# Optimization experiments

Measured on AMD Instinct MI355X. Metric: run time of the kernel, lower is better.

## Reference

```python
import jax, jax.numpy as jnp
import numpy as np

N_NODES = 50000

def _sage(x, src, dst, Wl, bl, Wr):
    # PyG SAGEConv(aggr='mean'): out = lin_l(mean_{j in N(i)} x_j) + lin_r(x_i)
    msg = x[src]                                                    # [E, F] gather
    agg = jax.ops.segment_sum(msg, dst, num_segments=N_NODES)      # [N, F]
    cnt = jax.ops.segment_sum(jnp.ones((src.shape[0],), x.dtype), dst, num_segments=N_NODES)
    agg = agg / jnp.maximum(cnt, 1.0)[:, None]                     # mean aggregate
    return agg @ Wl + bl + x @ Wr                                   # lin_l has bias, lin_r does not


def setup_inputs() -> dict:
    key = jax.random.key(0)
    ks = jax.random.split(key, 14)
    d_in, d_h, d_out, n_edges = 128, 64, 4, 800000
    s = lambda k, shp, fan: jax.random.normal(k, shp, jnp.float32) * (1.0 / np.sqrt(fan))
    return {
        'x': jax.random.normal(ks[0], (N_NODES, d_in), jnp.float32),
        'edge_index': jax.random.randint(ks[1], (2, n_edges), 0, N_NODES, jnp.int64),
        'Wl1': s(ks[2], (d_in, d_h), d_in), 'bl1': jnp.zeros((d_h,), jnp.float32),
        'Wr1': s(ks[3], (d_in, d_h), d_in),
        'Wl2': s(ks[4], (d_h, d_h), d_h), 'bl2': jnp.zeros((d_h,), jnp.float32),
        'Wr2': s(ks[5], (d_h, d_h), d_h),
        'Wl3': s(ks[6], (d_h, d_h), d_h), 'bl3': jnp.zeros((d_h,), jnp.float32),
        'Wr3': s(ks[7], (d_h, d_h), d_h),
        'Wp': s(ks[8], (2 * d_h, d_out), 2 * d_h), 'bp': jnp.zeros((d_out,), jnp.float32),
    }


def reference(x, edge_index, Wl1, bl1, Wr1, Wl2, bl2, Wr2, Wl3, bl3, Wr3, Wp, bp):
    src, dst = edge_index[0], edge_index[1]
    # dropout is identity in eval mode
    h = jax.nn.elu(_sage(x, src, dst, Wl1, bl1, Wr1))
    h = jax.nn.elu(_sage(h, src, dst, Wl2, bl2, Wr2))
    h = jax.nn.elu(_sage(h, src, dst, Wl3, bl3, Wr3))
    edge_feat = jnp.concatenate([h[src], h[dst]], axis=1)  # [E, 2*hidden]
    return edge_feat @ Wp + bp                              # [E, output_dim]
```

## Files before the change

kernel.cpp:

```cpp
#include <hip/hip_runtime.h>
#include <hip/hip_bf16.h>

#define N_NODES 50000
#define N_EDGES 800000
#define D_IN 128
#define D_H 64
#define SCAN_BLOCKS 196
#define HIST_BLOCKS 3125
#define LIN1_BLOCKS 782

#define F1L 0
#define F1R 8192
#define F2L 16384
#define F2R 20480
#define F3L 24576
#define F3R 28672
#define FRAG_TOTAL 32768

typedef short bf16x8 __attribute__((ext_vector_type(8)));
typedef float f32x4 __attribute__((ext_vector_type(4)));

__device__ __forceinline__ ushort f2bf(float f) {
    __hip_bfloat16 b = __float2bfloat16(f);
    return *reinterpret_cast<ushort*>(&b);
}
__device__ __forceinline__ float bf16_lo(unsigned int u) { return __uint_as_float(u << 16); }
__device__ __forceinline__ float bf16_hi(unsigned int u) { return __uint_as_float(u & 0xffff0000u); }

__device__ __forceinline__ void build_frag_one(const float* __restrict__ W, int local,
                                               ushort* __restrict__ frag, int fid) {
    int lane = local & 63;
    int ktnt = local >> 6;
    int kt = ktnt >> 2, nt = ktnt & 3;
    int quad = lane >> 4, col = lane & 15;
    ushort t0 = f2bf(W[(kt * 32 + quad * 8 + 0) * D_H + nt * 16 + col]);
    ushort t1 = f2bf(W[(kt * 32 + quad * 8 + 1) * D_H + nt * 16 + col]);
    ushort t2 = f2bf(W[(kt * 32 + quad * 8 + 2) * D_H + nt * 16 + col]);
    ushort t3 = f2bf(W[(kt * 32 + quad * 8 + 3) * D_H + nt * 16 + col]);
    ushort t4 = f2bf(W[(kt * 32 + quad * 8 + 4) * D_H + nt * 16 + col]);
    ushort t5 = f2bf(W[(kt * 32 + quad * 8 + 5) * D_H + nt * 16 + col]);
    ushort t6 = f2bf(W[(kt * 32 + quad * 8 + 6) * D_H + nt * 16 + col]);
    ushort t7 = f2bf(W[(kt * 32 + quad * 8 + 7) * D_H + nt * 16 + col]);
    uint4 v;
    v.x = (unsigned int)t0 | ((unsigned int)t1 << 16);
    v.y = (unsigned int)t2 | ((unsigned int)t3 << 16);
    v.z = (unsigned int)t4 | ((unsigned int)t5 << 16);
    v.w = (unsigned int)t6 | ((unsigned int)t7 << 16);
    *reinterpret_cast<uint4*>(frag + (size_t)fid * 8) = v;
}

__global__ void hist_frags_kernel(const int* __restrict__ dstv, int* __restrict__ cnt,
                                  ushort* __restrict__ rank,
                                  const float* __restrict__ Wl1, const float* __restrict__ Wr1,
                                  const float* __restrict__ Wl2, const float* __restrict__ Wr2,
                                  const float* __restrict__ Wl3, const float* __restrict__ Wr3,
                                  ushort* __restrict__ frag) {
    if (blockIdx.x < HIST_BLOCKS) {
        int e = blockIdx.x * 256 + threadIdx.x;
        if (e < N_EDGES) {
            int r = atomicAdd(&cnt[dstv[e]], 1);
            rank[e] = (ushort)r;
        }
    } else {
        int fid = (blockIdx.x - HIST_BLOCKS) * 256 + threadIdx.x;
        const float* W; int base;
        if (fid < 1024)      { W = Wl1; base = 0; }
        else if (fid < 2048) { W = Wr1; base = 1024; }
        else if (fid < 2560) { W = Wl2; base = 2048; }
        else if (fid < 3072) { W = Wr2; base = 2560; }
        else if (fid < 3584) { W = Wl3; base = 3072; }
        else                 { W = Wr3; base = 3584; }
        build_frag_one(W, fid - base, frag, fid);
    }
}

__global__ void scan_partial(const int* __restrict__ cnt, int* __restrict__ blockSums) {
    __shared__ int s[256];
    int i = blockIdx.x * 256 + threadIdx.x;
    s[threadIdx.x] = (i < N_NODES) ? cnt[i] : 0;
    __syncthreads();
    for (int off = 128; off > 0; off >>= 1) {
        if (threadIdx.x < off) s[threadIdx.x] += s[threadIdx.x + off];
        __syncthreads();
    }
    if (threadIdx.x == 0) blockSums[blockIdx.x] = s[0];
}

__global__ void scan_final(const int* __restrict__ cnt, const int* __restrict__ blockSums,
                           int* __restrict__ row_ptr) {
    __shared__ int s[256];
    __shared__ int bs[256];
    int t = threadIdx.x;
    bs[t] = (t < SCAN_BLOCKS) ? blockSums[t] : 0;
    int i = blockIdx.x * 256 + t;
    s[t] = (i < N_NODES) ? cnt[i] : 0;
    __syncthreads();
    for (int off = 1; off < 256; off <<= 1) {
        int tmp1 = (t >= off) ? s[t - off] : 0;
        int tmp2 = (t >= off) ? bs[t - off] : 0;
        __syncthreads();
        s[t] += tmp1;
        bs[t] += tmp2;
        __syncthreads();
    }
    int blockExcl = (blockIdx.x > 0) ? bs[blockIdx.x - 1] : 0;
    int excl = blockExcl + ((t > 0) ? s[t - 1] : 0);
    if (i < N_NODES) row_ptr[i] = excl;
    if (i == 0) row_ptr[N_NODES] = N_EDGES;
}

template <int FIN, bool BF16IN>
__device__ __forceinline__ void lin_body(int gwave, int lane, const void* __restrict__ hin,
                                         const ushort* __restrict__ fragWl,
                                         const ushort* __restrict__ fragWr,
                                         ushort* __restrict__ Y, ushort* __restrict__ Zb) {
    constexpr int KT = FIN / 32;
    int m0 = gwave * 16;
    if (m0 >= N_NODES) return;
    int col = lane & 15;
    int quad = lane >> 4;

    bf16x8 blf[KT][4], brf[KT][4];
#pragma unroll
    for (int kt = 0; kt < KT; ++kt)
#pragma unroll
        for (int nt = 0; nt < 4; ++nt) {
            size_t off = (size_t)((kt * 4 + nt) * 64 + lane) * 8;
            blf[kt][nt] = __builtin_bit_cast(bf16x8, *reinterpret_cast<const uint4*>(fragWl + off));
            brf[kt][nt] = __builtin_bit_cast(bf16x8, *reinterpret_cast<const uint4*>(fragWr + off));
        }

    f32x4 accl0 = {0.f,0.f,0.f,0.f}, accl1 = accl0, accl2 = accl0, accl3 = accl0;
    f32x4 accr0 = accl0, accr1 = accl0, accr2 = accl0, accr3 = accl0;
#pragma unroll
    for (int kt = 0; kt < KT; ++kt) {
        bf16x8 a;
        if (BF16IN) {
            const ushort* arow = (const ushort*)hin + (size_t)(m0 + col) * FIN + quad * 8;
            a = __builtin_bit_cast(bf16x8, *reinterpret_cast<const uint4*>(arow + kt * 32));
        } else {
            const float* arow = (const float*)hin + (size_t)(m0 + col) * FIN + quad * 8;
            float4 a_lo = *reinterpret_cast<const float4*>(arow + kt * 32);
            float4 a_hi = *reinterpret_cast<const float4*>(arow + kt * 32 + 4);
            a[0] = (short)f2bf(a_lo.x); a[1] = (short)f2bf(a_lo.y);
            a[2] = (short)f2bf(a_lo.z); a[3] = (short)f2bf(a_lo.w);
            a[4] = (short)f2bf(a_hi.x); a[5] = (short)f2bf(a_hi.y);
            a[6] = (short)f2bf(a_hi.z); a[7] = (short)f2bf(a_hi.w);
        }
        accl0 = __builtin_amdgcn_mfma_f32_16x16x32_bf16(a, blf[kt][0], accl0, 0, 0, 0);
        accl1 = __builtin_amdgcn_mfma_f32_16x16x32_bf16(a, blf[kt][1], accl1, 0, 0, 0);
        accl2 = __builtin_amdgcn_mfma_f32_16x16x32_bf16(a, blf[kt][2], accl2, 0, 0, 0);
        accl3 = __builtin_amdgcn_mfma_f32_16x16x32_bf16(a, blf[kt][3], accl3, 0, 0, 0);
        accr0 = __builtin_amdgcn_mfma_f32_16x16x32_bf16(a, brf[kt][0], accr0, 0, 0, 0);
        accr1 = __builtin_amdgcn_mfma_f32_16x16x32_bf16(a, brf[kt][1], accr1, 0, 0, 0);
        accr2 = __builtin_amdgcn_mfma_f32_16x16x32_bf16(a, brf[kt][2], accr2, 0, 0, 0);
        accr3 = __builtin_amdgcn_mfma_f32_16x16x32_bf16(a, brf[kt][3], accr3, 0, 0, 0);
    }
#pragma unroll
    for (int reg = 0; reg < 4; ++reg) {
        size_t r = (size_t)(m0 + quad * 4 + reg) * D_H;
        ushort* yp = Y + r;
        yp[0 * 16 + col] = f2bf(accl0[reg]);
        yp[1 * 16 + col] = f2bf(accl1[reg]);
        yp[2 * 16 + col] = f2bf(accl2[reg]);
        yp[3 * 16 + col] = f2bf(accl3[reg]);
        ushort* zp = Zb + r;
        zp[0 * 16 + col] = f2bf(accr0[reg]);
        zp[1 * 16 + col] = f2bf(accr1[reg]);
        zp[2 * 16 + col] = f2bf(accr2[reg]);
        zp[3 * 16 + col] = f2bf(accr3[reg]);
    }
}

__global__ void lin1_fill_kernel(const float* __restrict__ x, const ushort* __restrict__ wfrag,
                                 const int* __restrict__ srcv, const int* __restrict__ dstv,
                                 const ushort* __restrict__ rank, const int* __restrict__ row_ptr,
                                 ushort* __restrict__ csr_src,
                                 ushort* __restrict__ Y, ushort* __restrict__ Zb) {
    if (blockIdx.x < LIN1_BLOCKS) {
        int gwave = (blockIdx.x * 256 + threadIdx.x) >> 6;
        lin_body<D_IN, false>(gwave, threadIdx.x & 63, x, wfrag + F1L, wfrag + F1R, Y, Zb);
    } else {
        int e = (blockIdx.x - LIN1_BLOCKS) * 256 + threadIdx.x;
        if (e < N_EDGES) {
            int d = dstv[e];
            int pos = row_ptr[d] + (int)rank[e];
            csr_src[pos] = (ushort)srcv[e];
        }
    }
}

__global__ void linYZ_b_kernel(const ushort* __restrict__ hb, const ushort* __restrict__ fragWl,
                               const ushort* __restrict__ fragWr,
                               ushort* __restrict__ Y, ushort* __restrict__ Zb) {
    int gwave = (blockIdx.x * 256 + threadIdx.x) >> 6;
    lin_body<D_H, true>(gwave, threadIdx.x & 63, hb, fragWl, fragWr, Y, Zb);
}

template <bool FUSE_PROJ>
__global__ void gather_kernel(const ushort* __restrict__ Y, const ushort* __restrict__ Zb,
                              const float* __restrict__ bl,
                              const int* __restrict__ row_ptr, const ushort* __restrict__ csr_src,
                              ushort* __restrict__ outb,
                              const float* __restrict__ Wp,
                              float* __restrict__ ps, float* __restrict__ pd) {
    int wv = (blockIdx.x << 2) + (threadIdx.x >> 6);
    int lane = threadIdx.x & 63;
    int nA = wv << 1;
    if (nA >= N_NODES) return;
    int nB = nA + 1;
    int g = lane >> 4;
    int l = lane & 15;

    int rp0 = row_ptr[nA];
    int rp1 = row_ptr[nA + 1];
    int rp2 = row_ptr[nA + 2];
    int degA = rp1 - rp0, degB = rp2 - rp1;

    float a0A=0.f,a1A=0.f,a2A=0.f,a3A=0.f;
    float a0B=0.f,a1B=0.f,a2B=0.f,a3B=0.f;
    const uint2* __restrict__ Y2 = reinterpret_cast<const uint2*>(Y);
    int maxdeg = degA > degB ? degA : degB;

    for (int base = 0; base < maxdeg; base += 64) {
        int wendA = degA - base; if (wendA > 64) wendA = 64;
        int wendB = degB - base; if (wendB > 64) wendB = 64;
        int idxA = (int)csr_src[rp0 + base + lane];
        int idxB = (int)csr_src[rp1 + base + lane];
        int kmax = wendA > wendB ? wendA : wendB;
        for (int k = 0; k < kmax; k += 16) {
            int e0 = k + g, e1 = k + 4 + g, e2 = k + 8 + g, e3 = k + 12 + g;
            int sA0 = __shfl(idxA, e0), sA1 = __shfl(idxA, e1);
            int sA2 = __shfl(idxA, e2), sA3 = __shfl(idxA, e3);
            int sB0 = __shfl(idxB, e0), sB1 = __shfl(idxB, e1);
            int sB2 = __shfl(idxB, e2), sB3 = __shfl(idxB, e3);
            uint2 rA0 = Y2[sA0 * 16 + l], rA1 = Y2[sA1 * 16 + l];
            uint2 rA2 = Y2[sA2 * 16 + l], rA3 = Y2[sA3 * 16 + l];
            uint2 rB0 = Y2[sB0 * 16 + l], rB1 = Y2[sB1 * 16 + l];
            uint2 rB2 = Y2[sB2 * 16 + l], rB3 = Y2[sB3 * 16 + l];
            if (e0 < wendA) { a0A += bf16_lo(rA0.x); a1A += bf16_hi(rA0.x); a2A += bf16_lo(rA0.y); a3A += bf16_hi(rA0.y); }
            if (e1 < wendA) { a0A += bf16_lo(rA1.x); a1A += bf16_hi(rA1.x); a2A += bf16_lo(rA1.y); a3A += bf16_hi(rA1.y); }
            if (e2 < wendA) { a0A += bf16_lo(rA2.x); a1A += bf16_hi(rA2.x); a2A += bf16_lo(rA2.y); a3A += bf16_hi(rA2.y); }
            if (e3 < wendA) { a0A += bf16_lo(rA3.x); a1A += bf16_hi(rA3.x); a2A += bf16_lo(rA3.y); a3A += bf16_hi(rA3.y); }
            if (e0 < wendB) { a0B += bf16_lo(rB0.x); a1B += bf16_hi(rB0.x); a2B += bf16_lo(rB0.y); a3B += bf16_hi(rB0.y); }
            if (e1 < wendB) { a0B += bf16_lo(rB1.x); a1B += bf16_hi(rB1.x); a2B += bf16_lo(rB1.y); a3B += bf16_hi(rB1.y); }
            if (e2 < wendB) { a0B += bf16_lo(rB2.x); a1B += bf16_hi(rB2.x); a2B += bf16_lo(rB2.y); a3B += bf16_hi(rB2.y); }
            if (e3 < wendB) { a0B += bf16_lo(rB3.x); a1B += bf16_hi(rB3.x); a2B += bf16_lo(rB3.y); a3B += bf16_hi(rB3.y); }
        }
    }

    a0A += __shfl_xor(a0A, 16); a0A += __shfl_xor(a0A, 32);
    a1A += __shfl_xor(a1A, 16); a1A += __shfl_xor(a1A, 32);
    a2A += __shfl_xor(a2A, 16); a2A += __shfl_xor(a2A, 32);
    a3A += __shfl_xor(a3A, 16); a3A += __shfl_xor(a3A, 32);
    a0B += __shfl_xor(a0B, 16); a0B += __shfl_xor(a0B, 32);
    a1B += __shfl_xor(a1B, 16); a1B += __shfl_xor(a1B, 32);
    a2B += __shfl_xor(a2B, 16); a2B += __shfl_xor(a2B, 32);
    a3B += __shfl_xor(a3B, 16); a3B += __shfl_xor(a3B, 32);

    if (g < 2) {
        int node  = (g == 0) ? nA : nB;
        float dgf = (float)((g == 0) ? degA : degB);
        float inv = 1.0f / fmaxf(dgf, 1.0f);
        float c0 = (g == 0) ? a0A : a0B;
        float c1 = (g == 0) ? a1A : a1B;
        float c2 = (g == 0) ? a2A : a2B;
        float c3 = (g == 0) ? a3A : a3B;
        float4 bv = reinterpret_cast<const float4*>(bl)[l];
        uint2 zr = reinterpret_cast<const uint2*>(Zb)[node * 16 + l];
        float v0 = c0 * inv + bv.x + bf16_lo(zr.x);
        float v1 = c1 * inv + bv.y + bf16_hi(zr.x);
        float v2 = c2 * inv + bv.z + bf16_lo(zr.y);
        float v3 = c3 * inv + bv.w + bf16_hi(zr.y);
        float o0 = v0 > 0.f ? v0 : expm1f(v0);
        float o1 = v1 > 0.f ? v1 : expm1f(v1);
        float o2 = v2 > 0.f ? v2 : expm1f(v2);
        float o3 = v3 > 0.f ? v3 : expm1f(v3);

        if constexpr (!FUSE_PROJ) {
            ushort4 ob;
            ob.x = f2bf(o0); ob.y = f2bf(o1); ob.z = f2bf(o2); ob.w = f2bf(o3);
            reinterpret_cast<ushort4*>(outb)[node * 16 + l] = ob;
        } else {
            float p0 = 0.f, p1 = 0.f, p2 = 0.f, p3 = 0.f;
            float q0 = 0.f, q1 = 0.f, q2 = 0.f, q3 = 0.f;
            float ov[4] = {o0, o1, o2, o3};
#pragma unroll
            for (int j = 0; j < 4; ++j) {
                int k = 4 * l + j;
                float4 wt = reinterpret_cast<const float4*>(Wp)[k];
                float4 wb = reinterpret_cast<const float4*>(Wp)[D_H + k];
                p0 += ov[j] * wt.x; p1 += ov[j] * wt.y; p2 += ov[j] * wt.z; p3 += ov[j] * wt.w;
                q0 += ov[j] * wb.x; q1 += ov[j] * wb.y; q2 += ov[j] * wb.z; q3 += ov[j] * wb.w;
            }
#pragma unroll
            for (int off = 1; off < 16; off <<= 1) {
                p0 += __shfl_xor(p0, off); p1 += __shfl_xor(p1, off);
                p2 += __shfl_xor(p2, off); p3 += __shfl_xor(p3, off);
                q0 += __shfl_xor(q0, off); q1 += __shfl_xor(q1, off);
                q2 += __shfl_xor(q2, off); q3 += __shfl_xor(q3, off);
            }
            if (l == 0) {
                float4 pv; pv.x = p0; pv.y = p1; pv.z = p2; pv.w = p3;
                float4 qv; qv.x = q0; qv.y = q1; qv.z = q2; qv.w = q3;
                reinterpret_cast<float4*>(ps)[node] = pv;
                reinterpret_cast<float4*>(pd)[node] = qv;
            }
        }
    }
}

__global__ void edge_final_kernel(const int* __restrict__ srcv, const int* __restrict__ dstv,
                                  const float* __restrict__ ps, const float* __restrict__ pd,
                                  const float* __restrict__ bp, float* __restrict__ out) {
    int e = blockIdx.x * 256 + threadIdx.x;
    if (e >= N_EDGES) return;
    float4 a = reinterpret_cast<const float4*>(ps)[srcv[e]];
    float4 b = reinterpret_cast<const float4*>(pd)[dstv[e]];
    float4 o;
    o.x = a.x + b.x + bp[0];
    o.y = a.y + b.y + bp[1];
    o.z = a.z + b.z + bp[2];
    o.w = a.w + b.w + bp[3];
    reinterpret_cast<float4*>(out)[e] = o;
}

extern "C" void kernel_launch(void* const* d_in, const int* in_sizes, int n_in,
                              void* d_out, int out_size, void* d_ws, size_t ws_size,
                              hipStream_t stream) {
    const float* x   = (const float*)d_in[0];
    const int*   ei  = (const int*)d_in[1];
    const float* Wl1 = (const float*)d_in[2];
    const float* bl1 = (const float*)d_in[3];
    const float* Wr1 = (const float*)d_in[4];
    const float* Wl2 = (const float*)d_in[5];
    const float* bl2 = (const float*)d_in[6];
    const float* Wr2 = (const float*)d_in[7];
    const float* Wl3 = (const float*)d_in[8];
    const float* bl3 = (const float*)d_in[9];
    const float* Wr3 = (const float*)d_in[10];
    const float* Wp  = (const float*)d_in[11];
    const float* bp  = (const float*)d_in[12];
    float* out = (float*)d_out;

    const int* srcv = ei;
    const int* dstv = ei + N_EDGES;

    int*   cnt       = (int*)d_ws;
    int*   blockSums = cnt + 50000;
    int*   row_ptr   = blockSums + 256;
    ushort* rank     = (ushort*)(row_ptr + 50001);
    ushort* csr_src  = rank + 800000;
    ushort* wfrag = (ushort*)(((uintptr_t)(csr_src + 800064) + 127) & ~(uintptr_t)127);
    ushort* Y   = (ushort*)(((uintptr_t)(wfrag + FRAG_TOTAL) + 127) & ~(uintptr_t)127);
    ushort* Zb  = Y + (size_t)N_NODES * D_H;
    ushort* H1b = Zb + (size_t)N_NODES * D_H;
    ushort* H2b = H1b + (size_t)N_NODES * D_H;
    float* ps = (float*)(((uintptr_t)(H2b + (size_t)N_NODES * D_H) + 15) & ~(uintptr_t)15);
    float* pd = ps + (size_t)N_NODES * 4;

    hipMemsetAsync(cnt, 0, N_NODES * sizeof(int), stream);
    hist_frags_kernel<<<HIST_BLOCKS + 16, 256, 0, stream>>>(dstv, cnt, rank, Wl1, Wr1, Wl2, Wr2,
                                                            Wl3, Wr3, wfrag);
    scan_partial<<<SCAN_BLOCKS, 256, 0, stream>>>(cnt, blockSums);
    scan_final<<<SCAN_BLOCKS, 256, 0, stream>>>(cnt, blockSums, row_ptr);

    const int GATHER_GRID = N_NODES / 8;

    lin1_fill_kernel<<<LIN1_BLOCKS + HIST_BLOCKS, 256, 0, stream>>>(x, wfrag, srcv, dstv,
                                                                    rank, row_ptr, csr_src,
                                                                    Y, Zb);
    gather_kernel<false><<<GATHER_GRID, 256, 0, stream>>>(Y, Zb, bl1, row_ptr, csr_src, H1b,
                                                          nullptr, nullptr, nullptr);

    linYZ_b_kernel<<<LIN1_BLOCKS, 256, 0, stream>>>(H1b, wfrag + F2L, wfrag + F2R, Y, Zb);
    gather_kernel<false><<<GATHER_GRID, 256, 0, stream>>>(Y, Zb, bl2, row_ptr, csr_src, H2b,
                                                          nullptr, nullptr, nullptr);

    linYZ_b_kernel<<<LIN1_BLOCKS, 256, 0, stream>>>(H2b, wfrag + F3L, wfrag + F3R, Y, Zb);
    gather_kernel<true><<<GATHER_GRID, 256, 0, stream>>>(Y, Zb, bl3, row_ptr, csr_src, nullptr,
                                                         Wp, ps, pd);

    edge_final_kernel<<<(N_EDGES + 255) / 256, 256, 0, stream>>>(srcv, dstv, ps, pd, bp, out);
}
```

Baseline: 249.3 us.

## Fuse next-layer linear transform into gather kernel via shared-memory MFMA

Each gather block now handles 16 nodes (4 per wave) and, after the mean aggregation and ELU, stages the bf16 hidden rows in shared memory. It then runs the next layer's Wl/Wr MFMA projection in place, writing Y/Z for the next layer directly. This removes the separate linYZ kernels and the H1/H2 round trips through global memory. Y/Z buffers are ping-ponged between layers. The costs are a block-level sync, more register pressure from tracking 4 nodes per wave, and extra padding in csr_src reads, since the wave over-reads up to 64 entries past each row.

```diff
diff --git a/kernel.cpp b/kernel.cpp
--- a/kernel.cpp
+++ b/kernel.cpp
@@ -8,6 +8,7 @@
 #define SCAN_BLOCKS 196
 #define HIST_BLOCKS 3125
 #define LIN1_BLOCKS 782
+#define GL_BLOCKS 3125
 
 #define F1L 0
 #define F1R 8192
@@ -109,48 +110,43 @@
     if (i == 0) row_ptr[N_NODES] = N_EDGES;
 }
 
-template <int FIN, bool BF16IN>
-__device__ __forceinline__ void lin_body(int gwave, int lane, const void* __restrict__ hin,
-                                         const ushort* __restrict__ fragWl,
-                                         const ushort* __restrict__ fragWr,
-                                         ushort* __restrict__ Y, ushort* __restrict__ Zb) {
-    constexpr int KT = FIN / 32;
+__device__ __forceinline__ void lin1_body(int gwave, int lane, const float* __restrict__ hin,
+                                          const ushort* __restrict__ fragWl,
+                                          const ushort* __restrict__ fragWr,
+                                          ushort* __restrict__ Y, ushort* __restrict__ Zb) {
+    constexpr int KT = D_IN / 32;
     int m0 = gwave * 16;
     if (m0 >= N_NODES) return;
     int col = lane & 15;
     int quad = lane >> 4;
 
-    bf16x8 blf[KT][4], brf[KT][4];
+    bf16x8 blf[KT], brf[KT][4];
+    bf16x8 blf2[KT][4];
 #pragma unroll
     for (int kt = 0; kt < KT; ++kt)
 #pragma unroll
         for (int nt = 0; nt < 4; ++nt) {
             size_t off = (size_t)((kt * 4 + nt) * 64 + lane) * 8;
-            blf[kt][nt] = __builtin_bit_cast(bf16x8, *reinterpret_cast<const uint4*>(fragWl + off));
+            blf2[kt][nt] = __builtin_bit_cast(bf16x8, *reinterpret_cast<const uint4*>(fragWl + off));
             brf[kt][nt] = __builtin_bit_cast(bf16x8, *reinterpret_cast<const uint4*>(fragWr + off));
         }
 
     f32x4 accl0 = {0.f,0.f,0.f,0.f}, accl1 = accl0, accl2 = accl0, accl3 = accl0;
     f32x4 accr0 = accl0, accr1 = accl0, accr2 = accl0, accr3 = accl0;
+    const float* arow = hin + (size_t)(m0 + col) * D_IN + quad * 8;
 #pragma unroll
     for (int kt = 0; kt < KT; ++kt) {
+        float4 a_lo = *reinterpret_cast<const float4*>(arow + kt * 32);
+        float4 a_hi = *reinterpret_cast<const float4*>(arow + kt * 32 + 4);
         bf16x8 a;
-        if (BF16IN) {
-            const ushort* arow = (const ushort*)hin + (size_t)(m0 + col) * FIN + quad * 8;
-            a = __builtin_bit_cast(bf16x8, *reinterpret_cast<const uint4*>(arow + kt * 32));
-        } else {
-            const float* arow = (const float*)hin + (size_t)(m0 + col) * FIN + quad * 8;
-            float4 a_lo = *reinterpret_cast<const float4*>(arow + kt * 32);
-            float4 a_hi = *reinterpret_cast<const float4*>(arow + kt * 32 + 4);
-            a[0] = (short)f2bf(a_lo.x); a[1] = (short)f2bf(a_lo.y);
-            a[2] = (short)f2bf(a_lo.z); a[3] = (short)f2bf(a_lo.w);
-            a[4] = (short)f2bf(a_hi.x); a[5] = (short)f2bf(a_hi.y);
-            a[6] = (short)f2bf(a_hi.z); a[7] = (short)f2bf(a_hi.w);
-        }
-        accl0 = __builtin_amdgcn_mfma_f32_16x16x32_bf16(a, blf[kt][0], accl0, 0, 0, 0);
-        accl1 = __builtin_amdgcn_mfma_f32_16x16x32_bf16(a, blf[kt][1], accl1, 0, 0, 0);
-        accl2 = __builtin_amdgcn_mfma_f32_16x16x32_bf16(a, blf[kt][2], accl2, 0, 0, 0);
-        accl3 = __builtin_amdgcn_mfma_f32_16x16x32_bf16(a, blf[kt][3], accl3, 0, 0, 0);
+        a[0] = (short)f2bf(a_lo.x); a[1] = (short)f2bf(a_lo.y);
+        a[2] = (short)f2bf(a_lo.z); a[3] = (short)f2bf(a_lo.w);
+        a[4] = (short)f2bf(a_hi.x); a[5] = (short)f2bf(a_hi.y);
+        a[6] = (short)f2bf(a_hi.z); a[7] = (short)f2bf(a_hi.w);
+        accl0 = __builtin_amdgcn_mfma_f32_16x16x32_bf16(a, blf2[kt][0], accl0, 0, 0, 0);
+        accl1 = __builtin_amdgcn_mfma_f32_16x16x32_bf16(a, blf2[kt][1], accl1, 0, 0, 0);
+        accl2 = __builtin_amdgcn_mfma_f32_16x16x32_bf16(a, blf2[kt][2], accl2, 0, 0, 0);
+        accl3 = __builtin_amdgcn_mfma_f32_16x16x32_bf16(a, blf2[kt][3], accl3, 0, 0, 0);
         accr0 = __builtin_amdgcn_mfma_f32_16x16x32_bf16(a, brf[kt][0], accr0, 0, 0, 0);
         accr1 = __builtin_amdgcn_mfma_f32_16x16x32_bf16(a, brf[kt][1], accr1, 0, 0, 0);
         accr2 = __builtin_amdgcn_mfma_f32_16x16x32_bf16(a, brf[kt][2], accr2, 0, 0, 0);
@@ -179,7 +175,7 @@
                                  ushort* __restrict__ Y, ushort* __restrict__ Zb) {
     if (blockIdx.x < LIN1_BLOCKS) {
         int gwave = (blockIdx.x * 256 + threadIdx.x) >> 6;
-        lin_body<D_IN, false>(gwave, threadIdx.x & 63, x, wfrag + F1L, wfrag + F1R, Y, Zb);
+        lin1_body(gwave, threadIdx.x & 63, x, wfrag + F1L, wfrag + F1R, Y, Zb);
     } else {
         int e = (blockIdx.x - LIN1_BLOCKS) * 256 + threadIdx.x;
         if (e < N_EDGES) {
@@ -190,122 +186,152 @@
     }
 }
 
-__global__ void linYZ_b_kernel(const ushort* __restrict__ hb, const ushort* __restrict__ fragWl,
-                               const ushort* __restrict__ fragWr,
-                               ushort* __restrict__ Y, ushort* __restrict__ Zb) {
-    int gwave = (blockIdx.x * 256 + threadIdx.x) >> 6;
-    lin_body<D_H, true>(gwave, threadIdx.x & 63, hb, fragWl, fragWr, Y, Zb);
-}
-
 template <bool FUSE_PROJ>
-__global__ void gather_kernel(const ushort* __restrict__ Y, const ushort* __restrict__ Zb,
-                              const float* __restrict__ bl,
-                              const int* __restrict__ row_ptr, const ushort* __restrict__ csr_src,
-                              ushort* __restrict__ outb,
-                              const float* __restrict__ Wp,
-                              float* __restrict__ ps, float* __restrict__ pd) {
-    int wv = (blockIdx.x << 2) + (threadIdx.x >> 6);
+__global__ void gather_lin_kernel(const ushort* __restrict__ Y, const ushort* __restrict__ Zb,
+                                  const float* __restrict__ bl,
+                                  const int* __restrict__ row_ptr, const ushort* __restrict__ csr_src,
+                                  const ushort* __restrict__ fragWl, const ushort* __restrict__ fragWr,
+                                  ushort* __restrict__ Ynext, ushort* __restrict__ Zbnext,
+                                  const float* __restrict__ Wp,
+                                  float* __restrict__ ps, float* __restrict__ pd) {
+    __shared__ ushort Hs[16][72];
+    int w = threadIdx.x >> 6;
     int lane = threadIdx.x & 63;
-    int nA = wv << 1;
-    if (nA >= N_NODES) return;
-    int nB = nA + 1;
+    int wv = (blockIdx.x << 2) + w;
+    int n0 = wv << 2;
     int g = lane >> 4;
     int l = lane & 15;
 
-    int rp0 = row_ptr[nA];
-    int rp1 = row_ptr[nA + 1];
-    int rp2 = row_ptr[nA + 2];
-    int degA = rp1 - rp0, degB = rp2 - rp1;
-
-    float a0A=0.f,a1A=0.f,a2A=0.f,a3A=0.f;
-    float a0B=0.f,a1B=0.f,a2B=0.f,a3B=0.f;
+    int rp[5];
+#pragma unroll
+    for (int i = 0; i < 5; ++i) rp[i] = row_ptr[n0 + i];
+    int deg[4];
+#pragma unroll
+    for (int n = 0; n < 4; ++n) deg[n] = rp[n + 1] - rp[n];
+    int maxdeg = deg[0];
+#pragma unroll
+    for (int n = 1; n < 4; ++n) maxdeg = deg[n] > maxdeg ? deg[n] : maxdeg;
+
+    float acc[4][4] = {{0.f}};
     const uint2* __restrict__ Y2 = reinterpret_cast<const uint2*>(Y);
-    int maxdeg = degA > degB ? degA : degB;
 
     for (int base = 0; base < maxdeg; base += 64) {
-        int wendA = degA - base; if (wendA > 64) wendA = 64;
-        int wendB = degB - base; if (wendB > 64) wendB = 64;
-        int idxA = (int)csr_src[rp0 + base + lane];
-        int idxB = (int)csr_src[rp1 + base + lane];
-        int kmax = wendA > wendB ? wendA : wendB;
+        int idxv[4];
+#pragma unroll
+        for (int n = 0; n < 4; ++n) idxv[n] = (int)csr_src[rp[n] + base + lane];
+        int wend[4];
+#pragma unroll
+        for (int n = 0; n < 4; ++n) { wend[n] = deg[n] - base; if (wend[n] > 64) wend[n] = 64; }
+        int kmax = wend[0];
+#pragma unroll
+        for (int n = 1; n < 4; ++n) kmax = wend[n] > kmax ? wend[n] : kmax;
         for (int k = 0; k < kmax; k += 16) {
-            int e0 = k + g, e1 = k + 4 + g, e2 = k + 8 + g, e3 = k + 12 + g;
-            int sA0 = __shfl(idxA, e0), sA1 = __shfl(idxA, e1);
-            int sA2 = __shfl(idxA, e2), sA3 = __shfl(idxA, e3);
-            int sB0 = __shfl(idxB, e0), sB1 = __shfl(idxB, e1);
-            int sB2 = __shfl(idxB, e2), sB3 = __shfl(idxB, e3);
-            uint2 rA0 = Y2[sA0 * 16 + l], rA1 = Y2[sA1 * 16 + l];
-            uint2 rA2 = Y2[sA2 * 16 + l], rA3 = Y2[sA3 * 16 + l];
-            uint2 rB0 = Y2[sB0 * 16 + l], rB1 = Y2[sB1 * 16 + l];
-            uint2 rB2 = Y2[sB2 * 16 + l], rB3 = Y2[sB3 * 16 + l];
-            if (e0 < wendA) { a0A += bf16_lo(rA0.x); a1A += bf16_hi(rA0.x); a2A += bf16_lo(rA0.y); a3A += bf16_hi(rA0.y); }
-            if (e1 < wendA) { a0A += bf16_lo(rA1.x); a1A += bf16_hi(rA1.x); a2A += bf16_lo(rA1.y); a3A += bf16_hi(rA1.y); }
-            if (e2 < wendA) { a0A += bf16_lo(rA2.x); a1A += bf16_hi(rA2.x); a2A += bf16_lo(rA2.y); a3A += bf16_hi(rA2.y); }
-            if (e3 < wendA) { a0A += bf16_lo(rA3.x); a1A += bf16_hi(rA3.x); a2A += bf16_lo(rA3.y); a3A += bf16_hi(rA3.y); }
-            if (e0 < wendB) { a0B += bf16_lo(rB0.x); a1B += bf16_hi(rB0.x); a2B += bf16_lo(rB0.y); a3B += bf16_hi(rB0.y); }
-            if (e1 < wendB) { a0B += bf16_lo(rB1.x); a1B += bf16_hi(rB1.x); a2B += bf16_lo(rB1.y); a3B += bf16_hi(rB1.y); }
-            if (e2 < wendB) { a0B += bf16_lo(rB2.x); a1B += bf16_hi(rB2.x); a2B += bf16_lo(rB2.y); a3B += bf16_hi(rB2.y); }
-            if (e3 < wendB) { a0B += bf16_lo(rB3.x); a1B += bf16_hi(rB3.x); a2B += bf16_lo(rB3.y); a3B += bf16_hi(rB3.y); }
-        }
-    }
-
-    a0A += __shfl_xor(a0A, 16); a0A += __shfl_xor(a0A, 32);
-    a1A += __shfl_xor(a1A, 16); a1A += __shfl_xor(a1A, 32);
-    a2A += __shfl_xor(a2A, 16); a2A += __shfl_xor(a2A, 32);
-    a3A += __shfl_xor(a3A, 16); a3A += __shfl_xor(a3A, 32);
-    a0B += __shfl_xor(a0B, 16); a0B += __shfl_xor(a0B, 32);
-    a1B += __shfl_xor(a1B, 16); a1B += __shfl_xor(a1B, 32);
-    a2B += __shfl_xor(a2B, 16); a2B += __shfl_xor(a2B, 32);
-    a3B += __shfl_xor(a3B, 16); a3B += __shfl_xor(a3B, 32);
-
-    if (g < 2) {
-        int node  = (g == 0) ? nA : nB;
-        float dgf = (float)((g == 0) ? degA : degB);
-        float inv = 1.0f / fmaxf(dgf, 1.0f);
-        float c0 = (g == 0) ? a0A : a0B;
-        float c1 = (g == 0) ? a1A : a1B;
-        float c2 = (g == 0) ? a2A : a2B;
-        float c3 = (g == 0) ? a3A : a3B;
-        float4 bv = reinterpret_cast<const float4*>(bl)[l];
-        uint2 zr = reinterpret_cast<const uint2*>(Zb)[node * 16 + l];
-        float v0 = c0 * inv + bv.x + bf16_lo(zr.x);
-        float v1 = c1 * inv + bv.y + bf16_hi(zr.x);
-        float v2 = c2 * inv + bv.z + bf16_lo(zr.y);
-        float v3 = c3 * inv + bv.w + bf16_hi(zr.y);
-        float o0 = v0 > 0.f ? v0 : expm1f(v0);
-        float o1 = v1 > 0.f ? v1 : expm1f(v1);
-        float o2 = v2 > 0.f ? v2 : expm1f(v2);
-        float o3 = v3 > 0.f ? v3 : expm1f(v3);
-
-        if constexpr (!FUSE_PROJ) {
-            ushort4 ob;
-            ob.x = f2bf(o0); ob.y = f2bf(o1); ob.z = f2bf(o2); ob.w = f2bf(o3);
-            reinterpret_cast<ushort4*>(outb)[node * 16 + l] = ob;
-        } else {
-            float p0 = 0.f, p1 = 0.f, p2 = 0.f, p3 = 0.f;
-            float q0 = 0.f, q1 = 0.f, q2 = 0.f, q3 = 0.f;
-            float ov[4] = {o0, o1, o2, o3};
-#pragma unroll
-            for (int j = 0; j < 4; ++j) {
-                int k = 4 * l + j;
-                float4 wt = reinterpret_cast<const float4*>(Wp)[k];
-                float4 wb = reinterpret_cast<const float4*>(Wp)[D_H + k];
-                p0 += ov[j] * wt.x; p1 += ov[j] * wt.y; p2 += ov[j] * wt.z; p3 += ov[j] * wt.w;
-                q0 += ov[j] * wb.x; q1 += ov[j] * wb.y; q2 += ov[j] * wb.z; q3 += ov[j] * wb.w;
-            }
-#pragma unroll
-            for (int off = 1; off < 16; off <<= 1) {
-                p0 += __shfl_xor(p0, off); p1 += __shfl_xor(p1, off);
-                p2 += __shfl_xor(p2, off); p3 += __shfl_xor(p3, off);
-                q0 += __shfl_xor(q0, off); q1 += __shfl_xor(q1, off);
-                q2 += __shfl_xor(q2, off); q3 += __shfl_xor(q3, off);
-            }
-            if (l == 0) {
-                float4 pv; pv.x = p0; pv.y = p1; pv.z = p2; pv.w = p3;
-                float4 qv; qv.x = q0; qv.y = q1; qv.z = q2; qv.w = q3;
-                reinterpret_cast<float4*>(ps)[node] = pv;
-                reinterpret_cast<float4*>(pd)[node] = qv;
-            }
+            uint2 rr[4][4];
+#pragma unroll
+            for (int n = 0; n < 4; ++n)
+#pragma unroll
+                for (int j = 0; j < 4; ++j) {
+                    int s = __shfl(idxv[n], k + 4 * j + g);
+                    rr[n][j] = Y2[s * 16 + l];
+                }
+#pragma unroll
+            for (int n = 0; n < 4; ++n)
+#pragma unroll
+                for (int j = 0; j < 4; ++j) {
+                    if (k + 4 * j + g < wend[n]) {
+                        acc[n][0] += bf16_lo(rr[n][j].x); acc[n][1] += bf16_hi(rr[n][j].x);
+                        acc[n][2] += bf16_lo(rr[n][j].y); acc[n][3] += bf16_hi(rr[n][j].y);
+                    }
+                }
+        }
+    }
+
+#pragma unroll
+    for (int n = 0; n < 4; ++n)
+#pragma unroll
+        for (int f = 0; f < 4; ++f) {
+            acc[n][f] += __shfl_xor(acc[n][f], 16);
+            acc[n][f] += __shfl_xor(acc[n][f], 32);
+        }
+
+    int node = n0 + g;
+    float dgf = (g == 0) ? (float)deg[0] : (g == 1) ? (float)deg[1]
+              : (g == 2) ? (float)deg[2] : (float)deg[3];
+    float c0 = (g == 0) ? acc[0][0] : (g == 1) ? acc[1][0] : (g == 2) ? acc[2][0] : acc[3][0];
+    float c1 = (g == 0) ? acc[0][1] : (g == 1) ? acc[1][1] : (g == 2) ? acc[2][1] : acc[3][1];
+    float c2 = (g == 0) ? acc[0][2] : (g == 1) ? acc[1][2] : (g == 2) ? acc[2][2] : acc[3][2];
+    float c3 = (g == 0) ? acc[0][3] : (g == 1) ? acc[1][3] : (g == 2) ? acc[2][3] : acc[3][3];
+    float inv = 1.0f / fmaxf(dgf, 1.0f);
+    float4 bv = reinterpret_cast<const float4*>(bl)[l];
+    uint2 zr = reinterpret_cast<const uint2*>(Zb)[node * 16 + l];
+    float v0 = c0 * inv + bv.x + bf16_lo(zr.x);
+    float v1 = c1 * inv + bv.y + bf16_hi(zr.x);
+    float v2 = c2 * inv + bv.z + bf16_lo(zr.y);
+    float v3 = c3 * inv + bv.w + bf16_hi(zr.y);
+    float o0 = v0 > 0.f ? v0 : expm1f(v0);
+    float o1 = v1 > 0.f ? v1 : expm1f(v1);
+    float o2 = v2 > 0.f ? v2 : expm1f(v2);
+    float o3 = v3 > 0.f ? v3 : expm1f(v3);
+
+    if constexpr (FUSE_PROJ) {
+        float p0 = 0.f, p1 = 0.f, p2 = 0.f, p3 = 0.f;
+        float q0 = 0.f, q1 = 0.f, q2 = 0.f, q3 = 0.f;
+        float ov[4] = {o0, o1, o2, o3};
+#pragma unroll
+        for (int j = 0; j < 4; ++j) {
+            int k = 4 * l + j;
+            float4 wt = reinterpret_cast<const float4*>(Wp)[k];
+            float4 wb = reinterpret_cast<const float4*>(Wp)[D_H + k];
+            p0 += ov[j] * wt.x; p1 += ov[j] * wt.y; p2 += ov[j] * wt.z; p3 += ov[j] * wt.w;
+            q0 += ov[j] * wb.x; q1 += ov[j] * wb.y; q2 += ov[j] * wb.z; q3 += ov[j] * wb.w;
+        }
+#pragma unroll
+        for (int off = 1; off < 16; off <<= 1) {
+            p0 += __shfl_xor(p0, off); p1 += __shfl_xor(p1, off);
+            p2 += __shfl_xor(p2, off); p3 += __shfl_xor(p3, off);
+            q0 += __shfl_xor(q0, off); q1 += __shfl_xor(q1, off);
+            q2 += __shfl_xor(q2, off); q3 += __shfl_xor(q3, off);
+        }
+        if (l == 0) {
+            float4 pv; pv.x = p0; pv.y = p1; pv.z = p2; pv.w = p3;
+            float4 qv; qv.x = q0; qv.y = q1; qv.z = q2; qv.w = q3;
+            reinterpret_cast<float4*>(ps)[node] = pv;
+            reinterpret_cast<float4*>(pd)[node] = qv;
+        }
+    } else {
+        ushort4 ob;
+        ob.x = f2bf(o0); ob.y = f2bf(o1); ob.z = f2bf(o2); ob.w = f2bf(o3);
+        int localrow = w * 4 + g;
+        *reinterpret_cast<ushort4*>(&Hs[localrow][4 * l]) = ob;
+        __syncthreads();
+
+        int col = lane & 15;
+        int quad = lane >> 4;
+        bf16x8 blf0 = __builtin_bit_cast(bf16x8,
+            *reinterpret_cast<const uint4*>(fragWl + (size_t)((0 * 4 + w) * 64 + lane) * 8));
+        bf16x8 blf1 = __builtin_bit_cast(bf16x8,
+            *reinterpret_cast<const uint4*>(fragWl + (size_t)((1 * 4 + w) * 64 + lane) * 8));
+        bf16x8 brf0 = __builtin_bit_cast(bf16x8,
+            *reinterpret_cast<const uint4*>(fragWr + (size_t)((0 * 4 + w) * 64 + lane) * 8));
+        bf16x8 brf1 = __builtin_bit_cast(bf16x8,
+            *reinterpret_cast<const uint4*>(fragWr + (size_t)((1 * 4 + w) * 64 + lane) * 8));
+        bf16x8 a0 = __builtin_bit_cast(bf16x8,
+            *reinterpret_cast<const uint4*>(&Hs[col][quad * 8]));
+        bf16x8 a1 = __builtin_bit_cast(bf16x8,
+            *reinterpret_cast<const uint4*>(&Hs[col][32 + quad * 8]));
+        f32x4 accl = {0.f,0.f,0.f,0.f};
+        f32x4 accr = {0.f,0.f,0.f,0.f};
+        accl = __builtin_amdgcn_mfma_f32_16x16x32_bf16(a0, blf0, accl, 0, 0, 0);
+        accl = __builtin_amdgcn_mfma_f32_16x16x32_bf16(a1, blf1, accl, 0, 0, 0);
+        accr = __builtin_amdgcn_mfma_f32_16x16x32_bf16(a0, brf0, accr, 0, 0, 0);
+        accr = __builtin_amdgcn_mfma_f32_16x16x32_bf16(a1, brf1, accr, 0, 0, 0);
+
+        int n0base = blockIdx.x * 16;
+#pragma unroll
+        for (int reg = 0; reg < 4; ++reg) {
+            size_t r = (size_t)(n0base + quad * 4 + reg) * D_H + w * 16 + col;
+            Ynext[r]  = f2bf(accl[reg]);
+            Zbnext[r] = f2bf(accr[reg]);
         }
     }
 }
@@ -351,12 +377,12 @@
     int*   row_ptr   = blockSums + 256;
     ushort* rank     = (ushort*)(row_ptr + 50001);
     ushort* csr_src  = rank + 800000;
-    ushort* wfrag = (ushort*)(((uintptr_t)(csr_src + 800064) + 127) & ~(uintptr_t)127);
-    ushort* Y   = (ushort*)(((uintptr_t)(wfrag + FRAG_TOTAL) + 127) & ~(uintptr_t)127);
-    ushort* Zb  = Y + (size_t)N_NODES * D_H;
-    ushort* H1b = Zb + (size_t)N_NODES * D_H;
-    ushort* H2b = H1b + (size_t)N_NODES * D_H;
-    float* ps = (float*)(((uintptr_t)(H2b + (size_t)N_NODES * D_H) + 15) & ~(uintptr_t)15);
+    ushort* wfrag = (ushort*)(((uintptr_t)(csr_src + 800000 + 4096) + 127) & ~(uintptr_t)127);
+    ushort* Y1  = (ushort*)(((uintptr_t)(wfrag + FRAG_TOTAL) + 127) & ~(uintptr_t)127);
+    ushort* Zb1 = Y1 + (size_t)N_NODES * D_H;
+    ushort* Y2  = Zb1 + (size_t)N_NODES * D_H;
+    ushort* Zb2 = Y2 + (size_t)N_NODES * D_H;
+    float* ps = (float*)(((uintptr_t)(Zb2 + (size_t)N_NODES * D_H) + 15) & ~(uintptr_t)15);
     float* pd = ps + (size_t)N_NODES * 4;
 
     hipMemsetAsync(cnt, 0, N_NODES * sizeof(int), stream);
@@ -365,21 +391,21 @@
     scan_partial<<<SCAN_BLOCKS, 256, 0, stream>>>(cnt, blockSums);
     scan_final<<<SCAN_BLOCKS, 256, 0, stream>>>(cnt, blockSums, row_ptr);
 
-    const int GATHER_GRID = N_NODES / 8;
-
     lin1_fill_kernel<<<LIN1_BLOCKS + HIST_BLOCKS, 256, 0, stream>>>(x, wfrag, srcv, dstv,
                                                                     rank, row_ptr, csr_src,
-                                                                    Y, Zb);
-    gather_kernel<false><<<GATHER_GRID, 256, 0, stream>>>(Y, Zb, bl1, row_ptr, csr_src, H1b,
-                                                          nullptr, nullptr, nullptr);
-
-    linYZ_b_kernel<<<LIN1_BLOCKS, 256, 0, stream>>>(H1b, wfrag + F2L, wfrag + F2R, Y, Zb);
-    gather_kernel<false><<<GATHER_GRID, 256, 0, stream>>>(Y, Zb, bl2, row_ptr, csr_src, H2b,
-                                                          nullptr, nullptr, nullptr);
-
-    linYZ_b_kernel<<<LIN1_BLOCKS, 256, 0, stream>>>(H2b, wfrag + F3L, wfrag + F3R, Y, Zb);
-    gather_kernel<true><<<GATHER_GRID, 256, 0, stream>>>(Y, Zb, bl3, row_ptr, csr_src, nullptr,
-                                                         Wp, ps, pd);
+                                                                    Y1, Zb1);
+
+    gather_lin_kernel<false><<<GL_BLOCKS, 256, 0, stream>>>(Y1, Zb1, bl1, row_ptr, csr_src,
+                                                            wfrag + F2L, wfrag + F2R, Y2, Zb2,
+                                                            nullptr, nullptr, nullptr);
+
+    gather_lin_kernel<false><<<GL_BLOCKS, 256, 0, stream>>>(Y2, Zb2, bl2, row_ptr, csr_src,
+                                                            wfrag + F3L, wfrag + F3R, Y1, Zb1,
+                                                            nullptr, nullptr, nullptr);
+
+    gather_lin_kernel<true><<<GL_BLOCKS, 256, 0, stream>>>(Y1, Zb1, bl3, row_ptr, csr_src,
+                                                           nullptr, nullptr, nullptr, nullptr,
+                                                           Wp, ps, pd);
 
     edge_final_kernel<<<(N_EDGES + 255) / 256, 256, 0, stream>>>(srcv, dstv, ps, pd, bp, out);
 }
```

New measurement: 234.6 us. 1.06x faster.
